# Optimization experiments

Measured on AMD Instinct MI355X. Metric: run time of the kernel, lower is better.

Reference implementation:

```python
import jax, jax.numpy as jnp
import numpy as np
from jax.scipy.special import logsumexp

EPS = 0.1
MAX_ITER = 50
THRESH = 1e-9


def _cost_matrix(x, y, p=2):
    # |x_i - y_j|^p summed over feature dim -> (N, P1, P2)
    return jnp.sum(jnp.abs(x[:, :, None, :] - y[:, None, :, :]) ** p, axis=-1)


def _sinkhorn_uv(C, eps, max_iter):
    # Log-domain Sinkhorn iterations; C is treated as a constant (torch no_grad).
    N, P1, P2 = C.shape
    log_mu = jnp.log(jnp.full((N, P1), 1.0 / P1, C.dtype) + 1e-8)
    log_nu = jnp.log(jnp.full((N, P2), 1.0 / P2, C.dtype) + 1e-8)

    def M(u, v):
        return (-C + u[:, :, None] + v[:, None, :]) / eps

    def cond(state):
        u, v, err, it = state
        return jnp.logical_and(it < max_iter, err >= THRESH)

    def body(state):
        u, v, err, it = state
        u1 = u
        u = eps * (log_mu - logsumexp(M(u, v), axis=-1)) + u
        v = eps * (log_nu - logsumexp(M(u, v), axis=-2)) + v
        err = jnp.mean(jnp.sum(jnp.abs(u - u1), axis=-1))
        return (u, v, err, it + 1)

    u0 = jnp.zeros((N, P1), C.dtype)
    v0 = jnp.zeros((N, P2), C.dtype)
    u, v, _, _ = jax.lax.while_loop(cond, body, (u0, v0, jnp.inf, 0))
    return u, v


def setup_inputs() -> dict:
    key = jax.random.key(0)
    kx, ky = jax.random.split(key)
    x = jax.random.normal(kx, (4, 2048, 64), dtype=jnp.float32)
    y = jax.random.normal(ky, (4, 2048, 64), dtype=jnp.float32)
    return {"x": x, "y": y}


def reference(x, y):
    C = _cost_matrix(x, y)
    # u, v computed under no_grad in torch -> constants w.r.t. x, y
    U, V = _sinkhorn_uv(jax.lax.stop_gradient(C), EPS, MAX_ITER)
    pi = jnp.exp((-C + U[:, :, None] + V[:, None, :]) / EPS)
    cost = jnp.sum(pi * C, axis=(-2, -1))  # reduction='none' -> (N,)
    return (cost, pi, C)
```

## Files before the change

kernel.cpp:

```cpp
#include <hip/hip_runtime.h>
#include <math.h>

#define NB 4
#define P 2048
#define DF 64
#define EPS 0.1f
#define INV_EPS 10.0f
#define MAX_ITER 50
#define NBLK 512
#define TPB 512
#define TR 128
#define TC 128
#define SCALE 14.426950408889634f
#define C2N 0.069314718055994531f
#define RPF (NB * 16 * 16 * 128)
#define CPF (NB * 16 * 16 * 128)

typedef float vfloat4 __attribute__((ext_vector_type(4)));

#if __has_builtin(__builtin_amdgcn_exp2f)
#define EXP2(x) __builtin_amdgcn_exp2f(x)
#else
#define EXP2(x) exp2f(x)
#endif
#if __has_builtin(__builtin_amdgcn_logf)
#define LOG2(x) __builtin_amdgcn_logf(x)
#else
#define LOG2(x) log2f(x)
#endif

struct BuildMem { float xs[32 * 132]; float ys[32 * 132]; };
union IterBuf {
  float rin[16 * 132];
  float Ld[64 * 133];
  float cin[16 * 132];
};
struct SMem {
  union { BuildMem b; IterBuf ib; } u;
  float red[132];
  float vlds[2][132];
};

__device__ __forceinline__ void flag_store(unsigned* f, unsigned v) {
  __hip_atomic_store(f, v, __ATOMIC_RELAXED, __HIP_MEMORY_SCOPE_AGENT);
}
__device__ __forceinline__ unsigned flag_load(unsigned* f) {
  return __hip_atomic_load(f, __ATOMIC_RELAXED, __HIP_MEMORY_SCOPE_AGENT);
}
__device__ __forceinline__ void store_f2_agent(float* p, float a, float b) {
  unsigned long long bits =
      ((unsigned long long)__float_as_uint(b) << 32) | __float_as_uint(a);
  __hip_atomic_store((unsigned long long*)p, bits, __ATOMIC_RELAXED,
                     __HIP_MEMORY_SCOPE_AGENT);
}
__device__ __forceinline__ float2 load_f2_agent(const float* p) {
  unsigned long long bits = __hip_atomic_load((unsigned long long*)p,
      __ATOMIC_RELAXED, __HIP_MEMORY_SCOPE_AGENT);
  return make_float2(__uint_as_float((unsigned)bits),
                     __uint_as_float((unsigned)(bits >> 32)));
}
__device__ __forceinline__ void store_f_agent(float* p, float v) {
  __hip_atomic_store(p, v, __ATOMIC_RELAXED, __HIP_MEMORY_SCOPE_AGENT);
}

__device__ __forceinline__ void lse_merge(float& M, float& S, float om, float os) {
  float d = EXP2(-fabsf(M - om));
  float Sn = (M >= om) ? fmaf(os, d, S) : fmaf(S, d, os);
  M = fmaxf(M, om);
  S = Sn;
}

__device__ __forceinline__ void u_stage(
    int k, int t, int c8, int r0, int ti, int tj, int n,
    const float (&cr)[2][16], const float* vl,
    float* rpp, unsigned* rf_mine) {
  float vv[16];
#pragma unroll
  for (int i = 0; i < 16; ++i) vv[i] = vl[32 * (i >> 2) + 4 * c8 + (i & 3)];
  float Lr[2];
#pragma unroll
  for (int r = 0; r < 2; ++r) {
    float d[16];
    float m = -3.4e38f;
#pragma unroll
    for (int i = 0; i < 16; ++i) {
      d[i] = vv[i] - cr[r][i];
      m = fmaxf(m, d[i]);
    }
    m = fmaxf(m, __shfl_xor(m, 1));
    m = fmaxf(m, __shfl_xor(m, 2));
    m = fmaxf(m, __shfl_xor(m, 4));
    float s = 0.f;
#pragma unroll
    for (int i = 0; i < 16; ++i) s += EXP2(d[i] - m);
    s += __shfl_xor(s, 1);
    s += __shfl_xor(s, 2);
    s += __shfl_xor(s, 4);
    Lr[r] = m + LOG2(s);
  }
  if (c8 == 0)
    store_f2_agent(rpp + ((n * 16 + ti) * 16 + tj) * TR + r0, Lr[0], Lr[1]);
  __threadfence_block();
  __syncthreads();
  if (t == 0) flag_store(rf_mine, (unsigned)(k + 1));
}

__device__ __forceinline__ void row_merge(
    int k, int t, int r0, int ti, int n,
    float (&Ucr)[2], const float* rpp, unsigned* rfb, SMem& sm, float l2mu) {
  if (t < 16) {
    while (flag_load(rfb + t) < (unsigned)(k + 1)) __builtin_amdgcn_s_sleep(1);
  }
  __syncthreads();
  {
    const int idx = 4 * t;
    const int j = t >> 5, row = idx & 127;
    const float* src = rpp + (n * 16 + ti) * 2048 + idx;
    float2 a = load_f2_agent(src);
    float2 b2 = load_f2_agent(src + 2);
    *(float2*)&sm.u.ib.rin[j * 132 + row] = a;
    *(float2*)&sm.u.ib.rin[j * 132 + row + 2] = b2;
  }
  __syncthreads();
  {
    const int row = t >> 2, q = t & 3;
    float L0 = sm.u.ib.rin[(4 * q + 0) * 132 + row];
    float L1 = sm.u.ib.rin[(4 * q + 1) * 132 + row];
    float L2 = sm.u.ib.rin[(4 * q + 2) * 132 + row];
    float L3 = sm.u.ib.rin[(4 * q + 3) * 132 + row];
    float M = fmaxf(fmaxf(L0, L1), fmaxf(L2, L3));
    float S = EXP2(L0 - M) + EXP2(L1 - M) + EXP2(L2 - M) + EXP2(L3 - M);
    float Mo = __shfl_xor(M, 1), So = __shfl_xor(S, 1);
    lse_merge(M, S, Mo, So);
    Mo = __shfl_xor(M, 2); So = __shfl_xor(S, 2);
    lse_merge(M, S, Mo, So);
    if (q == 0) sm.red[row] = l2mu - (M + LOG2(S));
  }
  __syncthreads();
  Ucr[0] = sm.red[r0];
  Ucr[1] = sm.red[r0 + 1];
}

__device__ __forceinline__ void v_stage(
    int k, int t, int w, int gg, int c8, int ti, int tj, int n,
    const float (&cr)[2][16], const float (&Ucr)[2],
    float* cpp, unsigned* cf_mine, SMem& sm) {
  const int grp = 8 * w + gg;
#pragma unroll
  for (int i = 0; i < 16; ++i) {
    float a0 = Ucr[0] - cr[0][i];
    float a1 = Ucr[1] - cr[1][i];
    float pm = fmaxf(a0, a1);
    float ps = 1.f + EXP2(-fabsf(a0 - a1));
    sm.u.ib.Ld[grp * 133 + 32 * (i >> 2) + 4 * c8 + (i & 3)] = pm + LOG2(ps);
  }
  __syncthreads();
  {
    const int col = t >> 2, q = t & 3;
    float L[16];
#pragma unroll
    for (int z = 0; z < 16; ++z) L[z] = sm.u.ib.Ld[(16 * q + z) * 133 + col];
    float M = L[0];
#pragma unroll
    for (int z = 1; z < 16; ++z) M = fmaxf(M, L[z]);
    float S = 0.f;
#pragma unroll
    for (int z = 0; z < 16; ++z) S += EXP2(L[z] - M);
    float Mo = __shfl_xor(M, 1), So = __shfl_xor(S, 1);
    lse_merge(M, S, Mo, So);
    Mo = __shfl_xor(M, 2); So = __shfl_xor(S, 2);
    lse_merge(M, S, Mo, So);
    if (q == 0) sm.red[col] = M + LOG2(S);
  }
  __syncthreads();
  if (t < TC)
    store_f_agent(cpp + ((n * 16 + tj) * 16 + ti) * TC + t, sm.red[t]);
  __threadfence_block();
  __syncthreads();
  if (t == 0) flag_store(cf_mine, (unsigned)(k + 1));
}

__device__ __forceinline__ void col_merge(
    int k, int t, int tj, int n, float* vl,
    const float* cpp, unsigned* cfb, SMem& sm, float l2mu) {
  if (t < 16) {
    while (flag_load(cfb + t) < (unsigned)(k + 1)) __builtin_amdgcn_s_sleep(1);
  }
  __syncthreads();
  {
    const int idx = 4 * t;
    const int j = t >> 5, col = idx & 127;
    const float* src = cpp + (n * 16 + tj) * 2048 + idx;
    float2 a = load_f2_agent(src);
    float2 b2 = load_f2_agent(src + 2);
    *(float2*)&sm.u.ib.cin[j * 132 + col] = a;
    *(float2*)&sm.u.ib.cin[j * 132 + col + 2] = b2;
  }
  __syncthreads();
  {
    const int col = t >> 2, q = t & 3;
    float L0 = sm.u.ib.cin[(4 * q + 0) * 132 + col];
    float L1 = sm.u.ib.cin[(4 * q + 1) * 132 + col];
    float L2 = sm.u.ib.cin[(4 * q + 2) * 132 + col];
    float L3 = sm.u.ib.cin[(4 * q + 3) * 132 + col];
    float M = fmaxf(fmaxf(L0, L1), fmaxf(L2, L3));
    float S = EXP2(L0 - M) + EXP2(L1 - M) + EXP2(L2 - M) + EXP2(L3 - M);
    float Mo = __shfl_xor(M, 1), So = __shfl_xor(S, 1);
    lse_merge(M, S, Mo, So);
    Mo = __shfl_xor(M, 2); So = __shfl_xor(S, 2);
    lse_merge(M, S, Mo, So);
    if (q == 0) vl[col] = l2mu - (M + LOG2(S));
  }
  __syncthreads();
}

__global__ __launch_bounds__(TPB, 4) void sinkhorn_all(
    const float* __restrict__ x, const float* __restrict__ y,
    float* __restrict__ Cout, float* __restrict__ pi,
    float* __restrict__ cost, float* __restrict__ rp,
    float* __restrict__ cp, unsigned* __restrict__ flags, float l2mu) {
  __shared__ SMem sm;
  const int t = threadIdx.x;
  const int w = t >> 6;
  const int l = t & 63;
  const int gg = l >> 3;
  const int c8 = l & 7;
  const int b = blockIdx.x;
  const int g = b >> 8;
  const int idx = b & 255;
  const int ti = idx >> 4;
  const int tj = idx & 15;
  const int nA = 2 * g, nB = 2 * g + 1;
  const int r0 = 16 * w + 2 * gg;
  unsigned* rfA_mine = flags + (nA * 16 + ti) * 16 + tj;
  unsigned* rfB_mine = flags + (nB * 16 + ti) * 16 + tj;
  unsigned* rfA_band = flags + (nA * 16 + ti) * 16;
  unsigned* rfB_band = flags + (nB * 16 + ti) * 16;
  unsigned* cfA_mine = flags + 1024 + (nA * 16 + tj) * 16 + ti;
  unsigned* cfB_mine = flags + 1024 + (nB * 16 + tj) * 16 + ti;
  unsigned* cfA_band = flags + 1024 + (nA * 16 + tj) * 16;
  unsigned* cfB_band = flags + 1024 + (nB * 16 + tj) * 16;
  unsigned* ef = flags + 2048;

  float creg[2][2][16];
  float U[2][2];

#pragma unroll
  for (int c = 0; c < 2; ++c) {
    const int n = 2 * g + c;
    const size_t xyb = (size_t)n * P * DF;
#pragma unroll
    for (int r = 0; r < 2; ++r)
#pragma unroll
      for (int i = 0; i < 16; ++i) creg[c][r][i] = 0.f;
#pragma unroll
    for (int h = 0; h < 2; ++h) {
      __syncthreads();
      {
        const int cl = t >> 2, db = (t & 3) * 8;
        const float* xp = x + xyb + (size_t)(TR * ti + cl) * DF + 32 * h + db;
        float4 q0 = *(const float4*)(xp);
        float4 q1 = *(const float4*)(xp + 4);
        float* xs = sm.u.b.xs;
        xs[(db + 0) * 132 + cl] = q0.x; xs[(db + 1) * 132 + cl] = q0.y;
        xs[(db + 2) * 132 + cl] = q0.z; xs[(db + 3) * 132 + cl] = q0.w;
        xs[(db + 4) * 132 + cl] = q1.x; xs[(db + 5) * 132 + cl] = q1.y;
        xs[(db + 6) * 132 + cl] = q1.z; xs[(db + 7) * 132 + cl] = q1.w;
        const float* yp = y + xyb + (size_t)(TC * tj + cl) * DF + 32 * h + db;
        q0 = *(const float4*)(yp);
        q1 = *(const float4*)(yp + 4);
        float* ys = sm.u.b.ys;
        ys[(db + 0) * 132 + cl] = q0.x; ys[(db + 1) * 132 + cl] = q0.y;
        ys[(db + 2) * 132 + cl] = q0.z; ys[(db + 3) * 132 + cl] = q0.w;
        ys[(db + 4) * 132 + cl] = q1.x; ys[(db + 5) * 132 + cl] = q1.y;
        ys[(db + 6) * 132 + cl] = q1.z; ys[(db + 7) * 132 + cl] = q1.w;
      }
      __syncthreads();
#pragma unroll 4
      for (int dd = 0; dd < 32; ++dd) {
        float2 x2 = *(const float2*)&sm.u.b.xs[dd * 132 + r0];
#pragma unroll
        for (int cc = 0; cc < 4; ++cc) {
          float4 y4 = *(const float4*)&sm.u.b.ys[dd * 132 + 32 * cc + 4 * c8];
          float d0, d1;
          d0 = x2.x - y4.x; creg[c][0][4*cc+0] = fmaf(d0, d0, creg[c][0][4*cc+0]);
          d1 = x2.y - y4.x; creg[c][1][4*cc+0] = fmaf(d1, d1, creg[c][1][4*cc+0]);
          d0 = x2.x - y4.y; creg[c][0][4*cc+1] = fmaf(d0, d0, creg[c][0][4*cc+1]);
          d1 = x2.y - y4.y; creg[c][1][4*cc+1] = fmaf(d1, d1, creg[c][1][4*cc+1]);
          d0 = x2.x - y4.z; creg[c][0][4*cc+2] = fmaf(d0, d0, creg[c][0][4*cc+2]);
          d1 = x2.y - y4.z; creg[c][1][4*cc+2] = fmaf(d1, d1, creg[c][1][4*cc+2]);
          d0 = x2.x - y4.w; creg[c][0][4*cc+3] = fmaf(d0, d0, creg[c][0][4*cc+3]);
          d1 = x2.y - y4.w; creg[c][1][4*cc+3] = fmaf(d1, d1, creg[c][1][4*cc+3]);
        }
      }
    }
    const size_t cb = (size_t)n * P * P;
#pragma unroll
    for (int r = 0; r < 2; ++r) {
      const size_t rowb = cb + (size_t)(TR * ti + r0 + r) * P + TC * tj;
#pragma unroll
      for (int cc = 0; cc < 4; ++cc) {
        vfloat4 c4 = {creg[c][r][4*cc+0], creg[c][r][4*cc+1],
                      creg[c][r][4*cc+2], creg[c][r][4*cc+3]};
        __builtin_nontemporal_store(c4, (vfloat4*)(Cout + rowb + 32*cc + 4*c8));
        creg[c][r][4*cc+0] *= SCALE;
        creg[c][r][4*cc+1] *= SCALE;
        creg[c][r][4*cc+2] *= SCALE;
        creg[c][r][4*cc+3] *= SCALE;
      }
    }
  }
  __syncthreads();
  if (t < 132) { sm.vlds[0][t] = 0.f; sm.vlds[1][t] = 0.f; }
  __syncthreads();

  float* vlA = sm.vlds[0];
  float* vlB = sm.vlds[1];
  u_stage(0, t, c8, r0, ti, tj, nA, creg[0], vlA, rp + RPF, rfA_mine);
  u_stage(0, t, c8, r0, ti, tj, nB, creg[1], vlB, rp + RPF, rfB_mine);
#pragma unroll 1
  for (int k = 0; k < MAX_ITER; ++k) {
    const int pw = (k + 1) & 1;
    float* rpp = rp + pw * RPF;
    float* cpp = cp + pw * CPF;
    float* rpn = rp + (k & 1) * RPF;
    row_merge(k, t, r0, ti, nA, U[0], rpp, rfA_band, sm, l2mu);
    v_stage(k, t, w, gg, c8, ti, tj, nA, creg[0], U[0], cpp, cfA_mine, sm);
    row_merge(k, t, r0, ti, nB, U[1], rpp, rfB_band, sm, l2mu);
    v_stage(k, t, w, gg, c8, ti, tj, nB, creg[1], U[1], cpp, cfB_mine, sm);
    col_merge(k, t, tj, nA, vlA, cpp, cfA_band, sm, l2mu);
    if (k + 1 < MAX_ITER)
      u_stage(k + 1, t, c8, r0, ti, tj, nA, creg[0], vlA, rpn, rfA_mine);
    col_merge(k, t, tj, nB, vlB, cpp, cfB_band, sm, l2mu);
    if (k + 1 < MAX_ITER)
      u_stage(k + 1, t, c8, r0, ti, tj, nB, creg[1], vlB, rpn, rfB_mine);
  }

  if (t == 0) flag_store(&ef[b], 1u);
  {
    while (flag_load(&ef[t]) < 1u) __builtin_amdgcn_s_sleep(1);
  }
  __syncthreads();
#pragma unroll
  for (int c = 0; c < 2; ++c) {
    const int n = 2 * g + c;
    float vv[16];
#pragma unroll
    for (int i = 0; i < 16; ++i)
      vv[i] = sm.vlds[c][32 * (i >> 2) + 4 * c8 + (i & 3)];
    float csum = 0.f;
#pragma unroll
    for (int r = 0; r < 2; ++r) {
      const size_t rowb = (size_t)n * P * P + (size_t)(TR*ti + r0 + r) * P + TC*tj;
#pragma unroll
      for (int cc = 0; cc < 4; ++cc) {
        vfloat4 p4;
        p4.x = EXP2(U[c][r] + vv[4*cc+0] - creg[c][r][4*cc+0]);
        p4.y = EXP2(U[c][r] + vv[4*cc+1] - creg[c][r][4*cc+1]);
        p4.z = EXP2(U[c][r] + vv[4*cc+2] - creg[c][r][4*cc+2]);
        p4.w = EXP2(U[c][r] + vv[4*cc+3] - creg[c][r][4*cc+3]);
        csum += p4.x * creg[c][r][4*cc+0] + p4.y * creg[c][r][4*cc+1]
              + p4.z * creg[c][r][4*cc+2] + p4.w * creg[c][r][4*cc+3];
        __builtin_nontemporal_store(p4, (vfloat4*)(pi + rowb + 32*cc + 4*c8));
      }
    }
    float cs = csum * C2N;
#pragma unroll
    for (int off = 32; off; off >>= 1) cs += __shfl_xor(cs, off);
    if (l == 0) atomicAdd(cost + n, cs);
  }
}

__global__ __launch_bounds__(256) void build_c(const float* __restrict__ x,
                                               const float* __restrict__ y,
                                               float* __restrict__ C,
                                               float* __restrict__ CT) {
  __shared__ float xs[DF][68];
  __shared__ float ys[DF][68];
  const int n = blockIdx.z;
  const int i0 = blockIdx.y * 64, j0 = blockIdx.x * 64;
  const int t = threadIdx.x;
  const int lr = t >> 4, c4 = (t & 15) * 4;
  const size_t xb = (size_t)n * P * DF;
  for (int rr = lr; rr < 64; rr += 16) {
    float4 xv = *(const float4*)(x + xb + (size_t)(i0 + rr) * DF + c4);
    float4 yv = *(const float4*)(y + xb + (size_t)(j0 + rr) * DF + c4);
    xs[c4 + 0][rr] = xv.x; xs[c4 + 1][rr] = xv.y;
    xs[c4 + 2][rr] = xv.z; xs[c4 + 3][rr] = xv.w;
    ys[c4 + 0][rr] = yv.x; ys[c4 + 1][rr] = yv.y;
    ys[c4 + 2][rr] = yv.z; ys[c4 + 3][rr] = yv.w;
  }
  __syncthreads();
  const int ty = t >> 4, tx = t & 15;
  float acc[4][4];
#pragma unroll
  for (int e = 0; e < 4; ++e)
#pragma unroll
    for (int f = 0; f < 4; ++f) acc[e][f] = 0.f;
#pragma unroll 4
  for (int d = 0; d < DF; ++d) {
    float4 a4 = *(const float4*)&xs[d][4 * ty];
    float4 b4 = *(const float4*)&ys[d][4 * tx];
    float av[4] = {a4.x, a4.y, a4.z, a4.w};
    float bv[4] = {b4.x, b4.y, b4.z, b4.w};
#pragma unroll
    for (int e = 0; e < 4; ++e)
#pragma unroll
      for (int f = 0; f < 4; ++f) {
        float df = av[e] - bv[f];
        acc[e][f] = fmaf(df, df, acc[e][f]);
      }
  }
  const size_t cbase = (size_t)n * P * P;
#pragma unroll
  for (int e = 0; e < 4; ++e) {
    float4 v4 = make_float4(acc[e][0], acc[e][1], acc[e][2], acc[e][3]);
    *(float4*)(C + cbase + (size_t)(i0 + 4 * ty + e) * P + (j0 + 4 * tx)) = v4;
  }
#pragma unroll
  for (int f = 0; f < 4; ++f) {
    float4 v4 = make_float4(acc[0][f], acc[1][f], acc[2][f], acc[3][f]);
    *(float4*)(CT + cbase + (size_t)(j0 + 4 * tx + f) * P + (i0 + 4 * ty)) = v4;
  }
}

__global__ __launch_bounds__(256) void lse_pass(const float* __restrict__ M,
                                                const float* __restrict__ wv_,
                                                float* __restrict__ out,
                                                float log_w) {
  __shared__ float red[8];
  const int b = blockIdx.x;
  const int n = b >> 11;
  const int t = threadIdx.x;
  const float4* row = (const float4*)(M + (size_t)b * P);
  const float4* wv = (const float4*)(wv_ + (size_t)n * P);
  float4 c0 = row[t], c1 = row[t + 256];
  float4 w0 = wv[t], w1 = wv[t + 256];
  float a[8];
  a[0] = (w0.x - c0.x) * INV_EPS; a[1] = (w0.y - c0.y) * INV_EPS;
  a[2] = (w0.z - c0.z) * INV_EPS; a[3] = (w0.w - c0.w) * INV_EPS;
  a[4] = (w1.x - c1.x) * INV_EPS; a[5] = (w1.y - c1.y) * INV_EPS;
  a[6] = (w1.z - c1.z) * INV_EPS; a[7] = (w1.w - c1.w) * INV_EPS;
  float mx = a[0];
#pragma unroll
  for (int k = 1; k < 8; ++k) mx = fmaxf(mx, a[k]);
#pragma unroll
  for (int o = 32; o > 0; o >>= 1) mx = fmaxf(mx, __shfl_xor(mx, o));
  if ((t & 63) == 0) red[t >> 6] = mx;
  __syncthreads();
  mx = fmaxf(fmaxf(red[0], red[1]), fmaxf(red[2], red[3]));
  float s = 0.f;
#pragma unroll
  for (int k = 0; k < 8; ++k) s += __expf(a[k] - mx);
#pragma unroll
  for (int o = 32; o > 0; o >>= 1) s += __shfl_xor(s, o);
  if ((t & 63) == 0) red[4 + (t >> 6)] = s;
  __syncthreads();
  if (t == 0) {
    float S = red[4] + red[5] + red[6] + red[7];
    out[b] = EPS * (log_w - (mx + __logf(S)));
  }
}

__global__ __launch_bounds__(256) void final_pass(const float* __restrict__ C,
                                                  const float* __restrict__ u,
                                                  const float* __restrict__ v,
                                                  float* __restrict__ pi,
                                                  float* __restrict__ cost) {
  __shared__ float red[4];
  const int b = blockIdx.x;
  const int n = b >> 11;
  const int t = threadIdx.x;
  const float ui = u[b];
  const float4* row = (const float4*)(C + (size_t)b * P);
  const float4* vv = (const float4*)(v + (size_t)n * P);
  float4* prow = (float4*)(pi + (size_t)b * P);
  float local = 0.f;
#pragma unroll
  for (int h = 0; h < 2; ++h) {
    float4 c = row[t + 256 * h];
    float4 vw = vv[t + 256 * h];
    float4 p;
    p.x = __expf((ui + vw.x - c.x) * INV_EPS);
    p.y = __expf((ui + vw.y - c.y) * INV_EPS);
    p.z = __expf((ui + vw.z - c.z) * INV_EPS);
    p.w = __expf((ui + vw.w - c.w) * INV_EPS);
    prow[t + 256 * h] = p;
    local += p.x * c.x + p.y * c.y + p.z * c.z + p.w * c.w;
  }
#pragma unroll
  for (int o = 32; o > 0; o >>= 1) local += __shfl_xor(local, o);
  if ((t & 63) == 0) red[t >> 6] = local;
  __syncthreads();
  if (t == 0) {
    float S = red[0] + red[1] + red[2] + red[3];
    atomicAdd(cost + n, S);
  }
}

extern "C" void kernel_launch(void* const* d_in, const int* in_sizes, int n_in,
                              void* d_out, int out_size, void* d_ws, size_t ws_size,
                              hipStream_t stream) {
  const float* x = (const float*)d_in[0];
  const float* y = (const float*)d_in[1];
  float* cost = (float*)d_out;
  float* pi = cost + 4;
  float* C = pi + (size_t)NB * P * P;
  float* rp = pi;
  float* cp = pi + 2 * RPF;
  unsigned* flags = (unsigned*)d_ws;

  (void)hipMemsetAsync(cost, 0, NB * sizeof(float), stream);
  (void)hipMemsetAsync(flags, 0, 10240, stream);

  float lmu = logf(1.0f / (float)P + 1e-8f);
  float l2mu = log2f(1.0f / (float)P + 1e-8f);

  void* args[] = {(void*)&x, (void*)&y, (void*)&C, (void*)&pi,
                  (void*)&cost, (void*)&rp, (void*)&cp, (void*)&flags,
                  (void*)&l2mu};
  hipError_t err = hipLaunchCooperativeKernel((void*)sinkhorn_all, dim3(NBLK),
                                              dim3(TPB), args, 0, stream);
  if (err != hipSuccess) {
    float* u = (float*)d_ws;
    float* v = u + NB * P;
    (void)hipMemsetAsync(v, 0, NB * P * sizeof(float), stream);
    float* CT = pi;
    build_c<<<dim3(32, 32, 4), 256, 0, stream>>>(x, y, C, CT);
    for (int it = 0; it < MAX_ITER; ++it) {
      lse_pass<<<NB * P, 256, 0, stream>>>(C, v, u, lmu);
      lse_pass<<<NB * P, 256, 0, stream>>>(CT, u, v, lmu);
    }
    final_pass<<<NB * P, 256, 0, stream>>>(C, u, v, pi, cost);
  }
}
```

Measured before the change: 911.4 us.

## Process all four batches per block with 256 persistent blocks

The persistent kernel now launches 256 blocks, each owning one 128x128 tile for all four batch items, instead of 512 blocks covering two batches each. This halves the number of blocks taking part in the flag-based grid synchronisation and gives each block more independent work to interleave between waits. In exchange each thread holds twice as many cost values in registers, launch bounds drop to 2 blocks per SM, and occupancy and spill risk change. Fewer blocks may also leave some compute units idle.

```diff
diff --git a/kernel.cpp b/kernel.cpp
--- a/kernel.cpp
+++ b/kernel.cpp
@@ -7,7 +7,7 @@
 #define EPS 0.1f
 #define INV_EPS 10.0f
 #define MAX_ITER 50
-#define NBLK 512
+#define NBLK 256
 #define TPB 512
 #define TR 128
 #define TC 128
@@ -38,7 +38,7 @@
 struct SMem {
   union { BuildMem b; IterBuf ib; } u;
   float red[132];
-  float vlds[2][132];
+  float vlds[4][132];
 };
 
 __device__ __forceinline__ void flag_store(unsigned* f, unsigned v) {
@@ -214,7 +214,7 @@
   __syncthreads();
 }
 
-__global__ __launch_bounds__(TPB, 4) void sinkhorn_all(
+__global__ __launch_bounds__(TPB, 2) void sinkhorn_all(
     const float* __restrict__ x, const float* __restrict__ y,
     float* __restrict__ Cout, float* __restrict__ pi,
     float* __restrict__ cost, float* __restrict__ rp,
@@ -226,28 +226,17 @@
   const int gg = l >> 3;
   const int c8 = l & 7;
   const int b = blockIdx.x;
-  const int g = b >> 8;
-  const int idx = b & 255;
-  const int ti = idx >> 4;
-  const int tj = idx & 15;
-  const int nA = 2 * g, nB = 2 * g + 1;
+  const int ti = b >> 4;
+  const int tj = b & 15;
   const int r0 = 16 * w + 2 * gg;
-  unsigned* rfA_mine = flags + (nA * 16 + ti) * 16 + tj;
-  unsigned* rfB_mine = flags + (nB * 16 + ti) * 16 + tj;
-  unsigned* rfA_band = flags + (nA * 16 + ti) * 16;
-  unsigned* rfB_band = flags + (nB * 16 + ti) * 16;
-  unsigned* cfA_mine = flags + 1024 + (nA * 16 + tj) * 16 + ti;
-  unsigned* cfB_mine = flags + 1024 + (nB * 16 + tj) * 16 + ti;
-  unsigned* cfA_band = flags + 1024 + (nA * 16 + tj) * 16;
-  unsigned* cfB_band = flags + 1024 + (nB * 16 + tj) * 16;
   unsigned* ef = flags + 2048;
 
-  float creg[2][2][16];
-  float U[2][2];
-
-#pragma unroll
-  for (int c = 0; c < 2; ++c) {
-    const int n = 2 * g + c;
+  float creg[4][2][16];
+  float U[4][2];
+
+#pragma unroll
+  for (int c = 0; c < 4; ++c) {
+    const int n = c;
     const size_t xyb = (size_t)n * P * DF;
 #pragma unroll
     for (int r = 0; r < 2; ++r)
@@ -311,39 +300,48 @@
     }
   }
   __syncthreads();
-  if (t < 132) { sm.vlds[0][t] = 0.f; sm.vlds[1][t] = 0.f; }
-  __syncthreads();
-
-  float* vlA = sm.vlds[0];
-  float* vlB = sm.vlds[1];
-  u_stage(0, t, c8, r0, ti, tj, nA, creg[0], vlA, rp + RPF, rfA_mine);
-  u_stage(0, t, c8, r0, ti, tj, nB, creg[1], vlB, rp + RPF, rfB_mine);
+  if (t < 132) {
+    sm.vlds[0][t] = 0.f; sm.vlds[1][t] = 0.f;
+    sm.vlds[2][t] = 0.f; sm.vlds[3][t] = 0.f;
+  }
+  __syncthreads();
+
+#pragma unroll
+  for (int c = 0; c < 4; ++c) {
+    unsigned* rfm = flags + (c * 16 + ti) * 16 + tj;
+    u_stage(0, t, c8, r0, ti, tj, c, creg[c], sm.vlds[c], rp + RPF, rfm);
+  }
 #pragma unroll 1
   for (int k = 0; k < MAX_ITER; ++k) {
     const int pw = (k + 1) & 1;
     float* rpp = rp + pw * RPF;
     float* cpp = cp + pw * CPF;
     float* rpn = rp + (k & 1) * RPF;
-    row_merge(k, t, r0, ti, nA, U[0], rpp, rfA_band, sm, l2mu);
-    v_stage(k, t, w, gg, c8, ti, tj, nA, creg[0], U[0], cpp, cfA_mine, sm);
-    row_merge(k, t, r0, ti, nB, U[1], rpp, rfB_band, sm, l2mu);
-    v_stage(k, t, w, gg, c8, ti, tj, nB, creg[1], U[1], cpp, cfB_mine, sm);
-    col_merge(k, t, tj, nA, vlA, cpp, cfA_band, sm, l2mu);
-    if (k + 1 < MAX_ITER)
-      u_stage(k + 1, t, c8, r0, ti, tj, nA, creg[0], vlA, rpn, rfA_mine);
-    col_merge(k, t, tj, nB, vlB, cpp, cfB_band, sm, l2mu);
-    if (k + 1 < MAX_ITER)
-      u_stage(k + 1, t, c8, r0, ti, tj, nB, creg[1], vlB, rpn, rfB_mine);
+#pragma unroll
+    for (int c = 0; c < 4; ++c) {
+      unsigned* rfb = flags + (c * 16 + ti) * 16;
+      unsigned* cfm = flags + 1024 + (c * 16 + tj) * 16 + ti;
+      row_merge(k, t, r0, ti, c, U[c], rpp, rfb, sm, l2mu);
+      v_stage(k, t, w, gg, c8, ti, tj, c, creg[c], U[c], cpp, cfm, sm);
+    }
+#pragma unroll
+    for (int c = 0; c < 4; ++c) {
+      unsigned* cfb = flags + 1024 + (c * 16 + tj) * 16;
+      unsigned* rfm = flags + (c * 16 + ti) * 16 + tj;
+      col_merge(k, t, tj, c, sm.vlds[c], cpp, cfb, sm, l2mu);
+      if (k + 1 < MAX_ITER)
+        u_stage(k + 1, t, c8, r0, ti, tj, c, creg[c], sm.vlds[c], rpn, rfm);
+    }
   }
 
   if (t == 0) flag_store(&ef[b], 1u);
-  {
+  if (t < NBLK) {
     while (flag_load(&ef[t]) < 1u) __builtin_amdgcn_s_sleep(1);
   }
   __syncthreads();
 #pragma unroll
-  for (int c = 0; c < 2; ++c) {
-    const int n = 2 * g + c;
+  for (int c = 0; c < 4; ++c) {
+    const int n = c;
     float vv[16];
 #pragma unroll
     for (int i = 0; i < 16; ++i)
```

New measurement: 1.174 ms. 1.29x slower.
